# Kernel tuning notes

Measured on AMD Instinct MI355X. Metric: run time of the kernel, lower is better.

## Reference

```python
import jax, jax.numpy as jnp
import numpy as np

DIM = 192          # out_dim
HEADS = 8          # num_heads (split into 2 branches of 4)
SS = (4, 8)        # split_size
B, HH, WW, CIN = 8, 128, 128, 192


def calc_mask(H, W, wh, ww):
    # Swin-style shift mask for windows of (wh, ww), shift (wh//2, ww//2).
    sh, sw = wh // 2, ww // 2
    h = jnp.arange(H)
    w = jnp.arange(W)
    hreg = (h >= H - wh).astype(jnp.int32) + (h >= H - sh).astype(jnp.int32)
    wreg = (w >= W - ww).astype(jnp.int32) + (w >= W - sw).astype(jnp.int32)
    img = hreg[:, None] * 3 + wreg[None, :]                      # (H, W) region ids
    win = img.reshape(H // wh, wh, W // ww, ww).transpose(0, 2, 1, 3).reshape(-1, wh * ww)
    return jnp.where(win[:, :, None] != win[:, None, :], -100.0, 0.0)  # (nW, N, N)


def window_attention(q, k, v, mask, d, Hsp, Wsp):
    # q,k,v: (B, C, H, W); mask: (u*v, N, N); d heads, window Hsp x Wsp
    Bc, C, H, W = k.shape
    u, vv = H // Hsp, W // Wsp
    c = C // d
    N = Hsp * Wsp
    scale = c ** -0.5

    def v2w(t):  # 'b (d c) (u h) (v w) -> (b u v) d (h w) c'
        return t.reshape(Bc, d, c, u, Hsp, vv, Wsp).transpose(0, 3, 5, 1, 4, 6, 2).reshape(Bc * u * vv, d, N, c)

    qw, kw, vw = v2w(q), v2w(k), v2w(v)
    attn = jnp.einsum('ndic,ndjc->ndij', qw, kw) * scale          # (B*u*v, d, N, N)
    attn = attn.reshape(Bc, u * vv, d, N, N) + mask[None, :, None, :, :]
    a = jax.nn.softmax(attn, axis=-1).reshape(Bc * u * vv, d, N, N)
    o = jnp.einsum('ndij,ndjc->ndic', a, vw)
    # '(b u v) d (h w) c -> b (d c) (u h) (v w)'
    return o.reshape(Bc, u, vv, d, Hsp, Wsp, c).transpose(0, 3, 6, 1, 4, 2, 5).reshape(Bc, C, H, W)


def setup_inputs() -> dict:
    key = jax.random.key(0)
    k0, k1, k2, k3 = jax.random.split(key, 4)
    x = jax.random.normal(k0, (B, HH * WW, CIN), dtype=jnp.float32)
    Wq = jax.random.normal(k1, (CIN, DIM), dtype=jnp.float32) * 0.02
    Wkv = jax.random.normal(k2, (CIN, 2 * DIM), dtype=jnp.float32) * 0.02
    Wproj = jax.random.normal(k3, (DIM, DIM), dtype=jnp.float32) * 0.02
    bproj = jnp.zeros((DIM,), dtype=jnp.float32)
    return {"x": x, "Wq": Wq, "Wkv": Wkv, "Wproj": Wproj, "bproj": bproj, "H": HH, "W": WW}


def reference(x, Wq, Wkv, Wproj, bproj, H, W):
    Bc, L, _ = x.shape
    C = Wq.shape[1]
    q = (x @ Wq).reshape(Bc, H, W, C).transpose(0, 3, 1, 2)       # (B, C, H, W)
    kv = (x @ Wkv).reshape(Bc, H, W, 2, C)
    k = kv[..., 0, :].transpose(0, 3, 1, 2)
    v = kv[..., 1, :].transpose(0, 3, 1, 2)

    Ch = C // 2
    s0, s1 = SS[0] // 2, SS[1] // 2
    roll0 = lambda t: jnp.roll(t, (-s0, -s1), axis=(-2, -1))
    roll1 = lambda t: jnp.roll(t, (-s1, -s0), axis=(-2, -1))
    mask0 = calc_mask(H, W, SS[0], SS[1])   # branch 0: 4x8 windows
    mask1 = calc_mask(H, W, SS[1], SS[0])   # branch 1: 8x4 windows
    d = HEADS // 2

    x0 = window_attention(roll0(q[:, :Ch]), roll0(k[:, :Ch]), roll0(v[:, :Ch]), mask0, d, SS[0], SS[1])
    x1 = window_attention(roll1(q[:, Ch:]), roll1(k[:, Ch:]), roll1(v[:, Ch:]), mask1, d, SS[1], SS[0])
    x0 = jnp.roll(x0, (s0, s1), axis=(-2, -1))
    x1 = jnp.roll(x1, (s1, s0), axis=(-2, -1))

    out = jnp.concatenate([x0, x1], axis=1)                        # (B, C, H, W)
    out = out.transpose(0, 2, 3, 1).reshape(Bc, L, C)
    return out @ Wproj + bproj
```

## Files before the change

kernel.cpp:

```cpp
#include <hip/hip_runtime.h>
#include <hip/hip_bf16.h>
#include <stdint.h>

typedef __bf16 bf16;
typedef __bf16 bf16x8 __attribute__((ext_vector_type(8)));
typedef __bf16 bf16x4 __attribute__((ext_vector_type(4)));
typedef float  f32x4  __attribute__((ext_vector_type(4)));

#define MROWS 131072

__device__ __forceinline__ f32x4 mfma16(bf16x8 a, bf16x8 b, f32x4 c) {
    return __builtin_amdgcn_mfma_f32_16x16x32_bf16(a, b, c, 0, 0, 0);
}
__device__ __forceinline__ f32x4 zero4() {
    f32x4 z; z[0]=0.f; z[1]=0.f; z[2]=0.f; z[3]=0.f; return z;
}
__device__ __forceinline__ bf16x8 zero8() {
    bf16x8 z;
#pragma unroll
    for (int i = 0; i < 8; ++i) z[i] = (bf16)0.f;
    return z;
}

__global__ void kw_transpose(const float* __restrict__ Wq, const float* __restrict__ Wkv,
                             const float* __restrict__ Wp, bf16* __restrict__ Wt,
                             bf16* __restrict__ Wpt) {
    int col = blockIdx.x;
    int k = threadIdx.x;
    if (col < 192)      Wt[col * 192 + k] = (bf16)Wq[k * 192 + col];
    else if (col < 576) Wt[col * 192 + k] = (bf16)Wkv[k * 384 + (col - 192)];
    else                Wpt[(col - 576) * 192 + k] = (bf16)Wp[k * 192 + (col - 576)];
}

__global__ __launch_bounds__(256, 4) void kfused(const float* __restrict__ X,
                                                 const bf16* __restrict__ Wt,
                                                 bf16* __restrict__ Out) {
    const int branch = blockIdx.y;
    const int bw = blockIdx.x;
    const int img = bw >> 9;
    const int widx = bw & 511;
    const int wh = branch ? 8 : 4, ww = branch ? 4 : 8;
    const int lww = branch ? 2 : 3;
    const int lnv = branch ? 5 : 4;
    const int sh = wh >> 1, sw = ww >> 1;
    const int wa = widx >> lnv;
    const int wb = widx & ((128 >> lww) - 1);

    __shared__ __align__(16) char smem[33792];
    bf16 (*xs)[200]    = (bf16(*)[200])smem;
    bf16 (*pl)[32][40] = (bf16(*)[32][40])smem;
    bf16 (*qs)[104]    = (bf16(*)[104])(smem + 12800);
    bf16 (*ob)[104]    = (bf16(*)[104])(smem + 12800);
    bf16 (*kss)[104]   = (bf16(*)[104])(smem + 19456);
    bf16 (*vt)[24][40] = (bf16(*)[24][40])(smem + 26112);
    __shared__ int pix[32];
    __shared__ int rid[32];

    const int tid = threadIdx.x;
    if (tid < 32) {
        int ih = tid >> lww, iw = tid & (ww - 1);
        int hh = wa * wh + ih, wp = wb * ww + iw;
        int hreg = (hh >= 128 - wh) + (hh >= 128 - sh);
        int wreg = (wp >= 128 - ww) + (wp >= 128 - sw);
        rid[tid] = hreg * 3 + wreg;
        int srh = (hh + sh) & 127, srw = (wp + sw) & 127;
        pix[tid] = img * 16384 + srh * 128 + srw;
    }

#pragma unroll
    for (int i = 0; i < 6; ++i) {
        int c = tid + i * 256;
        int row = c / 48, c4 = (c % 48) * 4;
        int ih = row >> lww, iw = row & (ww - 1);
        int hh = wa * wh + ih, wp = wb * ww + iw;
        int srh = (hh + sh) & 127, srw = (wp + sw) & 127;
        size_t px = (size_t)(img * 16384 + srh * 128 + srw);
        f32x4 f = *(const f32x4*)(X + px * 192 + c4);
        bf16x4 h;
#pragma unroll
        for (int e = 0; e < 4; ++e) h[e] = (bf16)f[e];
        *(bf16x4*)&xs[row][c4] = h;
    }
    __syncthreads();

    const int hd = tid >> 6;
    const int l = tid & 63, li = l & 15, lk = l >> 4;

    bf16x8 xf[2][6];
#pragma unroll
    for (int mt = 0; mt < 2; ++mt)
#pragma unroll
        for (int ks = 0; ks < 6; ++ks)
            xf[mt][ks] = *(const bf16x8*)&xs[mt * 16 + li][ks * 32 + lk * 8];

#define LOADW(dst, nt) {                                                            \
        int seg_ = (nt) / 6, cwi_ = ((nt) % 6) * 16;                                \
        const bf16* wr = Wt + (size_t)(seg_ * 192 + branch * 96 + cwi_ + li) * 192  \
                            + lk * 8;                                               \
        _Pragma("unroll")                                                           \
        for (int ks = 0; ks < 6; ++ks) dst[ks] = *(const bf16x8*)(wr + ks * 32);    \
    }
#define MFMA_SCATTER(frag, nt) {                                                    \
        f32x4 a0 = zero4(), a1 = zero4();                                           \
        _Pragma("unroll")                                                           \
        for (int ks = 0; ks < 6; ++ks) {                                            \
            a0 = mfma16(frag[ks], xf[0][ks], a0);                                   \
            a1 = mfma16(frag[ks], xf[1][ks], a1);                                   \
        }                                                                           \
        int seg_ = (nt) / 6, cwi_ = ((nt) % 6) * 16;                                \
        if (seg_ < 2) {                                                             \
            bf16 (*dst)[104] = (seg_ == 0) ? qs : kss;                              \
            bf16x4 p0, p1;                                                          \
            _Pragma("unroll")                                                       \
            for (int r = 0; r < 4; ++r) { p0[r] = (bf16)a0[r]; p1[r] = (bf16)a1[r]; } \
            *(bf16x4*)&dst[li][cwi_ + lk * 4] = p0;                                 \
            *(bf16x4*)&dst[16 + li][cwi_ + lk * 4] = p1;                            \
        } else {                                                                    \
            _Pragma("unroll")                                                       \
            for (int r = 0; r < 4; ++r) {                                           \
                int vc = cwi_ + lk * 4 + r;                                         \
                vt[vc / 24][vc % 24][li] = (bf16)a0[r];                             \
                vt[vc / 24][vc % 24][16 + li] = (bf16)a1[r];                        \
            }                                                                       \
        }                                                                           \
    }

    {
        bf16x8 cur[6], nxt[6];
        LOADW(cur, hd);
#pragma unroll
        for (int j = 0; j < 4; ++j) {
            int nt = hd + 4 * j;
            if (j < 3) {
                LOADW(nxt, nt + 4);
            } else if (hd < 2) {
                LOADW(nxt, nt + 4);
            }
            MFMA_SCATTER(cur, nt);
#pragma unroll
            for (int ks = 0; ks < 6; ++ks) cur[ks] = nxt[ks];
        }
        if (hd < 2) {
            MFMA_SCATTER(cur, hd + 16);
        }
    }
    __syncthreads();

    bf16x8 aq[2], bk[2];
#pragma unroll
    for (int t = 0; t < 2; ++t) {
        if (lk < 3) {
            aq[t] = *(const bf16x8*)&qs[t * 16 + li][hd * 24 + lk * 8];
            bk[t] = *(const bf16x8*)&kss[t * 16 + li][hd * 24 + lk * 8];
        } else {
            aq[t] = zero8();
            bk[t] = zero8();
        }
    }
    f32x4 s[2][2];
#pragma unroll
    for (int it = 0; it < 2; ++it)
#pragma unroll
        for (int jt = 0; jt < 2; ++jt) s[it][jt] = mfma16(aq[it], bk[jt], zero4());

    const float scale = 0.2041241452319315f;
    const int r0 = lk * 4;
    const int rj0 = rid[li], rj1 = rid[16 + li];
#pragma unroll
    for (int it = 0; it < 2; ++it) {
#pragma unroll
        for (int r = 0; r < 4; ++r) {
            int i = it * 16 + r0 + r;
            int ri = rid[i];
            float v0 = s[it][0][r] * scale + ((ri != rj0) ? -100.f : 0.f);
            float v1 = s[it][1][r] * scale + ((ri != rj1) ? -100.f : 0.f);
            float m = fmaxf(v0, v1);
#pragma unroll
            for (int d = 1; d < 16; d <<= 1) m = fmaxf(m, __shfl_xor(m, d));
            float e0 = __expf(v0 - m), e1 = __expf(v1 - m);
            float sm = e0 + e1;
#pragma unroll
            for (int d = 1; d < 16; d <<= 1) sm += __shfl_xor(sm, d);
            float inv = 1.f / sm;
            pl[hd][i][li] = (bf16)(e0 * inv);
            pl[hd][i][16 + li] = (bf16)(e1 * inv);
        }
    }
    __syncthreads();

    bf16x8 ap[2], bv[2];
#pragma unroll
    for (int it = 0; it < 2; ++it)
        ap[it] = *(const bf16x8*)(&pl[hd][it * 16 + li][lk * 8]);
#pragma unroll
    for (int ct = 0; ct < 2; ++ct) {
        int col = ct * 16 + li;
        if (col > 23) col = 23;
        bv[ct] = *(const bf16x8*)(&vt[hd][col][lk * 8]);
    }
    f32x4 o[2][2];
#pragma unroll
    for (int it = 0; it < 2; ++it)
#pragma unroll
        for (int ct = 0; ct < 2; ++ct) o[it][ct] = mfma16(ap[it], bv[ct], zero4());

#pragma unroll
    for (int it = 0; it < 2; ++it)
#pragma unroll
        for (int ct = 0; ct < 2; ++ct) {
            int col = ct * 16 + li;
            if (col < 24) {
#pragma unroll
                for (int r = 0; r < 4; ++r)
                    ob[it * 16 + r0 + r][hd * 24 + col] = (bf16)o[it][ct][r];
            }
        }
    __syncthreads();
    for (int c = tid; c < 384; c += 256) {
        int row = c / 12, ch = c % 12;
        *(bf16x8*)(Out + (size_t)pix[row] * 192 + branch * 96 + ch * 8) =
            *(const bf16x8*)&ob[row][ch * 8];
    }
#undef LOADW
#undef MFMA_SCATTER
}

#define BSTR 200
__global__ __launch_bounds__(256, 4) void kproj(const bf16* __restrict__ Ab,
                                                const bf16* __restrict__ Wpt,
                                                const float* __restrict__ bias,
                                                float* __restrict__ Out) {
    __shared__ __align__(16) bf16 Bs[96][BSTR];
    const int lid = blockIdx.x;
    const int xcd = lid & 7, s = lid >> 3;
    const int mg = xcd * 128 + s / 2;
    const int nb = s & 1;
    const int tid = threadIdx.x;
    const int w = tid >> 6, l = tid & 63, li = l & 15, lk = l >> 4;
    const int rb = mg * 128 + w * 32;
    const int cb = nb * 96;

    bf16x8 a[2][6];
#pragma unroll
    for (int it = 0; it < 2; ++it)
#pragma unroll
        for (int ks = 0; ks < 6; ++ks)
            a[it][ks] = *(const bf16x8*)(Ab + (size_t)(rb + it * 16 + li) * 192 + ks * 32 + lk * 8);

#pragma unroll
    for (int i = 0; i < 9; ++i) {
        int c = i * 256 + tid;
        int r = c / 24, col = (c % 24) * 8;
        *(bf16x8*)&Bs[r][col] = *(const bf16x8*)(Wpt + (size_t)(cb + r) * 192 + col);
    }
    __syncthreads();

    f32x4 acc[2][6];
#pragma unroll
    for (int it = 0; it < 2; ++it)
#pragma unroll
        for (int nt = 0; nt < 6; ++nt) acc[it][nt] = zero4();

#pragma unroll
    for (int nt = 0; nt < 6; ++nt) {
#pragma unroll
        for (int ks = 0; ks < 6; ++ks) {
            bf16x8 b = *(const bf16x8*)&Bs[nt * 16 + li][ks * 32 + lk * 8];
            acc[0][nt] = mfma16(b, a[0][ks], acc[0][nt]);
            acc[1][nt] = mfma16(b, a[1][ks], acc[1][nt]);
        }
    }

#pragma unroll
    for (int nt = 0; nt < 6; ++nt) {
        f32x4 bv4 = *(const f32x4*)(bias + cb + nt * 16 + lk * 4);
#pragma unroll
        for (int it = 0; it < 2; ++it) {
            f32x4 ov = acc[it][nt];
#pragma unroll
            for (int r = 0; r < 4; ++r) ov[r] += bv4[r];
            *(f32x4*)(Out + (size_t)(rb + it * 16 + li) * 192 + cb + nt * 16 + lk * 4) = ov;
        }
    }
}

extern "C" void kernel_launch(void* const* d_in, const int* in_sizes, int n_in,
                              void* d_out, int out_size, void* d_ws, size_t ws_size,
                              hipStream_t stream) {
    const float* x    = (const float*)d_in[0];
    const float* Wq   = (const float*)d_in[1];
    const float* Wkv  = (const float*)d_in[2];
    const float* Wp   = (const float*)d_in[3];
    const float* bias = (const float*)d_in[4];
    float* out = (float*)d_out;

    bf16* Ab  = (bf16*)d_ws;
    bf16* Wt  = Ab + (size_t)MROWS * 192;
    bf16* Wpt = Wt + 576 * 192;

    hipLaunchKernelGGL(kw_transpose, dim3(768), dim3(192), 0, stream, Wq, Wkv, Wp, Wt, Wpt);
    hipLaunchKernelGGL(kfused, dim3(4096, 2), dim3(256), 0, stream, x, Wt, Ab);
    hipLaunchKernelGGL(kproj, dim3(2048), dim3(256), 0, stream, Ab, Wpt, bias, out);
}
```

Before: 148.2 us.

## Alias K buffer over X tile, raise occupancy, use DPP row reductions

Places the K staging buffer over the X tile in shared memory, which cuts LDS per block so the launch bound can ask for 5 blocks per CU instead of 4. To make the aliasing safe, W fragments are loaded into registers and a barrier is added before the projection writes, plus another barrier after the QK MFMAs so the softmax probabilities can overwrite K. The softmax max and sum reductions switch from shfl_xor to DPP row_ror moves, and the X load loop now steps row and column indices incrementally instead of dividing. The extra barriers and the tighter register budget may cost some of what the added occupancy gains.

```diff
diff --git a/kernel.cpp b/kernel.cpp
--- a/kernel.cpp
+++ b/kernel.cpp
@@ -20,6 +20,25 @@
 #pragma unroll
     for (int i = 0; i < 8; ++i) z[i] = (bf16)0.f;
     return z;
+}
+template <int CTRL>
+__device__ __forceinline__ float rowror(float x) {
+    return __int_as_float(
+        __builtin_amdgcn_mov_dpp(__float_as_int(x), CTRL, 0xF, 0xF, false));
+}
+__device__ __forceinline__ float rowmax16(float m) {
+    m = fmaxf(m, rowror<0x128>(m));
+    m = fmaxf(m, rowror<0x124>(m));
+    m = fmaxf(m, rowror<0x122>(m));
+    m = fmaxf(m, rowror<0x121>(m));
+    return m;
+}
+__device__ __forceinline__ float rowsum16(float s) {
+    s += rowror<0x128>(s);
+    s += rowror<0x124>(s);
+    s += rowror<0x122>(s);
+    s += rowror<0x121>(s);
+    return s;
 }
 
 __global__ void kw_transpose(const float* __restrict__ Wq, const float* __restrict__ Wkv,
@@ -32,7 +51,7 @@
     else                Wpt[(col - 576) * 192 + k] = (bf16)Wp[k * 192 + (col - 576)];
 }
 
-__global__ __launch_bounds__(256, 4) void kfused(const float* __restrict__ X,
+__global__ __launch_bounds__(256, 5) void kfused(const float* __restrict__ X,
                                                  const bf16* __restrict__ Wt,
                                                  bf16* __restrict__ Out) {
     const int branch = blockIdx.y;
@@ -46,13 +65,13 @@
     const int wa = widx >> lnv;
     const int wb = widx & ((128 >> lww) - 1);
 
-    __shared__ __align__(16) char smem[33792];
+    __shared__ __align__(16) char smem[27136];
     bf16 (*xs)[200]    = (bf16(*)[200])smem;
+    bf16 (*kss)[104]   = (bf16(*)[104])smem;
     bf16 (*pl)[32][40] = (bf16(*)[32][40])smem;
     bf16 (*qs)[104]    = (bf16(*)[104])(smem + 12800);
     bf16 (*ob)[104]    = (bf16(*)[104])(smem + 12800);
-    bf16 (*kss)[104]   = (bf16(*)[104])(smem + 19456);
-    bf16 (*vt)[24][40] = (bf16(*)[24][40])(smem + 26112);
+    bf16 (*vt)[24][40] = (bf16(*)[24][40])(smem + 19456);
     __shared__ int pix[32];
     __shared__ int rid[32];
 
@@ -67,19 +86,22 @@
         pix[tid] = img * 16384 + srh * 128 + srw;
     }
 
-#pragma unroll
-    for (int i = 0; i < 6; ++i) {
-        int c = tid + i * 256;
-        int row = c / 48, c4 = (c % 48) * 4;
-        int ih = row >> lww, iw = row & (ww - 1);
-        int hh = wa * wh + ih, wp = wb * ww + iw;
-        int srh = (hh + sh) & 127, srw = (wp + sw) & 127;
-        size_t px = (size_t)(img * 16384 + srh * 128 + srw);
-        f32x4 f = *(const f32x4*)(X + px * 192 + c4);
-        bf16x4 h;
-#pragma unroll
-        for (int e = 0; e < 4; ++e) h[e] = (bf16)f[e];
-        *(bf16x4*)&xs[row][c4] = h;
+    {
+        int row = tid / 48, rem = tid % 48;
+#pragma unroll
+        for (int i = 0; i < 6; ++i) {
+            int c4 = rem * 4;
+            int ih = row >> lww, iw = row & (ww - 1);
+            int hh = wa * wh + ih, wp = wb * ww + iw;
+            int srh = (hh + sh) & 127, srw = (wp + sw) & 127;
+            f32x4 f = *(const f32x4*)(X + (size_t)(img * 16384 + srh * 128 + srw) * 192 + c4);
+            bf16x4 h;
+#pragma unroll
+            for (int e = 0; e < 4; ++e) h[e] = (bf16)f[e];
+            *(bf16x4*)&xs[row][c4] = h;
+            row += 5; rem += 16;
+            if (rem >= 48) { rem -= 48; ++row; }
+        }
     }
     __syncthreads();
 
@@ -125,24 +147,24 @@
         }                                                                           \
     }
 
-    {
-        bf16x8 cur[6], nxt[6];
-        LOADW(cur, hd);
-#pragma unroll
-        for (int j = 0; j < 4; ++j) {
-            int nt = hd + 4 * j;
-            if (j < 3) {
-                LOADW(nxt, nt + 4);
-            } else if (hd < 2) {
-                LOADW(nxt, nt + 4);
-            }
-            MFMA_SCATTER(cur, nt);
-#pragma unroll
-            for (int ks = 0; ks < 6; ++ks) cur[ks] = nxt[ks];
-        }
-        if (hd < 2) {
-            MFMA_SCATTER(cur, hd + 16);
-        }
+    bf16x8 cur[6], nxt[6];
+    LOADW(cur, hd);
+    __syncthreads();
+
+#pragma unroll
+    for (int j = 0; j < 4; ++j) {
+        int nt = hd + 4 * j;
+        if (j < 3) {
+            LOADW(nxt, nt + 4);
+        } else if (hd < 2) {
+            LOADW(nxt, nt + 4);
+        }
+        MFMA_SCATTER(cur, nt);
+#pragma unroll
+        for (int ks = 0; ks < 6; ++ks) cur[ks] = nxt[ks];
+    }
+    if (hd < 2) {
+        MFMA_SCATTER(cur, hd + 16);
     }
     __syncthreads();
 
@@ -163,6 +185,8 @@
 #pragma unroll
         for (int jt = 0; jt < 2; ++jt) s[it][jt] = mfma16(aq[it], bk[jt], zero4());
 
+    __syncthreads();
+
     const float scale = 0.2041241452319315f;
     const int r0 = lk * 4;
     const int rj0 = rid[li], rj1 = rid[16 + li];
@@ -174,13 +198,9 @@
             int ri = rid[i];
             float v0 = s[it][0][r] * scale + ((ri != rj0) ? -100.f : 0.f);
             float v1 = s[it][1][r] * scale + ((ri != rj1) ? -100.f : 0.f);
-            float m = fmaxf(v0, v1);
-#pragma unroll
-            for (int d = 1; d < 16; d <<= 1) m = fmaxf(m, __shfl_xor(m, d));
+            float m = rowmax16(fmaxf(v0, v1));
             float e0 = __expf(v0 - m), e1 = __expf(v1 - m);
-            float sm = e0 + e1;
-#pragma unroll
-            for (int d = 1; d < 16; d <<= 1) sm += __shfl_xor(sm, d);
+            float sm = rowsum16(e0 + e1);
             float inv = 1.f / sm;
             pl[hd][i][li] = (bf16)(e0 * inv);
             pl[hd][i][16 + li] = (bf16)(e1 * inv);
```

After: 246.9 us. 66.7% more time.
